# Optimization experiments

Hardware: AMD Instinct MI355X
Metric: run time of the kernel (lower is better)

The kernel has to match this reference:

```python
import jax, jax.numpy as jnp
import numpy as np

B, N, D = 8, 2048, 1024
A_STDP, TAU_STDP, W_OFF, T_MAX = 0.9, 0.5, 0.9, 1.0
V_TH, EPS = 1.0, 1e-5


def setup_inputs() -> dict:
    key = jax.random.key(0)
    ks = jax.random.split(key, 6)
    s = 0.02
    inp = {"x": jax.random.normal(ks[0], (B, N, D), dtype=jnp.float32)}
    for i, nm in enumerate(["q", "k", "v"]):
        inp[f"W{nm}"] = jax.random.normal(ks[1 + i], (D, D), dtype=jnp.float32) * s
        inp[f"g{nm}"] = jnp.ones((D,), jnp.float32)
        inp[f"b{nm}"] = jnp.zeros((D,), jnp.float32)
        inp[f"m{nm}"] = jnp.zeros((D,), jnp.float32)
        inp[f"v{nm}"] = jnp.ones((D,), jnp.float32)
    inp["Wo"] = jax.random.normal(ks[4], (D, D), dtype=jnp.float32) * s
    inp["bo"] = jnp.zeros((D,), jnp.float32)
    return inp


def _proj(x, W, g, b, m, v):
    # Linear (no bias) -> BatchNorm1d (inference, running stats) -> LIF first step
    h = x @ W                                     # [B,N,D]
    h = (h - m) * (g * jax.lax.rsqrt(v + EPS)) + b
    # LIF with mem=None: mem = x, spike = sigmoid(4*(mem - v_th))
    return jax.nn.sigmoid(4.0 * (h - V_TH))


def reference(x, Wq, gq, bq, mq, vq, Wk, gk, bk, mk, vk, Wv, gv, bv, mv, vv, Wo, bo):
    Q = _proj(x, Wq, gq, bq, mq, vq)
    K = _proj(x, Wk, gk, bk, mk, vk)
    V = _proj(x, Wv, gv, bv, mv, vv)
    t_Q = T_MAX * (1.0 - Q.mean(axis=-1, keepdims=True))   # [B,N,1]
    t_K = T_MAX * (1.0 - K.mean(axis=-1, keepdims=True))   # [B,N,1]
    delta_t = t_Q - jnp.swapaxes(t_K, 1, 2)                 # [B,N,N]
    f_stdp = A_STDP * jnp.exp(-jnp.abs(delta_t) / TAU_STDP)
    A = jnp.where(delta_t < 0, f_stdp, -f_stdp) + W_OFF     # [B,N,N]
    return (A @ V) @ Wo + bo                                # [B,N,D]
```

## Files before the change

kernel.cpp:

```cpp
#include <hip/hip_runtime.h>

#define B_ 8
#define N_ 2048
#define D_ 1024
#define M_ (B_*N_)
#define SEGS 64
#define EPB (4096/SEGS)
#define CW 256

typedef __attribute__((ext_vector_type(8))) short short8;
typedef __attribute__((ext_vector_type(4))) float floatx4;

__device__ __forceinline__ ushort f2bf(float f) {
  unsigned u = __builtin_bit_cast(unsigned, f);
  return (ushort)((u + 0x7fffu + ((u >> 16) & 1u)) >> 16);
}
__device__ __forceinline__ float bf2f(ushort u) {
  return __builtin_bit_cast(float, ((unsigned)u) << 16);
}
__device__ __forceinline__ void gload16(const void* g, void* l) {
  __builtin_amdgcn_global_load_lds(
      (const __attribute__((address_space(1))) unsigned*)g,
      (__attribute__((address_space(3))) unsigned*)l, 16, 0, 0);
}
__device__ __forceinline__ float sig4(float h) {
  return 1.0f / (1.0f + __expf(4.0f - 4.0f*h));
}

__global__ __launch_bounds__(256) void conv_x_k(const float4* __restrict__ x,
                                                ushort4* __restrict__ o) {
  int i = blockIdx.x * 256 + threadIdx.x;
  float4 f = x[i];
  ushort4 u;
  u.x = f2bf(f.x); u.y = f2bf(f.y); u.z = f2bf(f.z); u.w = f2bf(f.w);
  o[i] = u;
}

__global__ __launch_bounds__(256) void transpose_k(
    const float* __restrict__ Wq, const float* __restrict__ Wk,
    const float* __restrict__ Wv, const float* __restrict__ Wo,
    ushort* __restrict__ W3T, ushort* __restrict__ WoT) {
  __shared__ float tile[32][33];
  int z = blockIdx.z;
  const float* W = (z == 0) ? Wq : (z == 1) ? Wk : (z == 2) ? Wv : Wo;
  ushort* WT = (z < 3) ? (W3T + (size_t)z * D_ * D_) : WoT;
  int tx = threadIdx.x, ty = threadIdx.y;
  int x = blockIdx.x * 32 + tx;
  int y = blockIdx.y * 32 + ty;
#pragma unroll
  for (int j = 0; j < 32; j += 8)
    tile[ty + j][tx] = W[(size_t)(y + j) * D_ + x];
  __syncthreads();
  int x2 = blockIdx.y * 32 + tx;
  int y2 = blockIdx.x * 32 + ty;
#pragma unroll
  for (int j = 0; j < 32; j += 8)
    WT[(size_t)(y2 + j) * D_ + x2] = f2bf(tile[tx][ty + j]);
}

__device__ __forceinline__ void mainloop256(
    const ushort* __restrict__ Ab, const ushort* __restrict__ Bb,
    ushort* __restrict__ As, ushort* __restrict__ Bs, int t,
    floatx4 (&acc)[8][4])
{
  const int lane = t & 63, wid = t >> 6;
  const int quad = lane >> 4, l15 = lane & 15;
  const int wm = wid >> 2, wn = wid & 3;

  int srcO[2], dsto[2];
#pragma unroll
  for (int r = 0; r < 2; r++) {
    int li = r * 512 + t;
    int row = li >> 2, c = li & 3;
    int soff = ((c - (row >> 1)) & 3) * 8;
    srcO[r] = row * D_ + soff;
    dsto[r] = li * 16;
  }

  int offA[8], offB[4];
#pragma unroll
  for (int i = 0; i < 8; i++) {
    int row = wm * 128 + i * 16 + l15;
    offA[i] = row * 32 + ((quad + (row >> 1)) & 3) * 8;
  }
#pragma unroll
  for (int i = 0; i < 4; i++) {
    int row = wn * 64 + i * 16 + l15;
    offB[i] = row * 32 + ((quad + (row >> 1)) & 3) * 8;
  }

#pragma unroll
  for (int pt = 0; pt < 3; pt++) {
#pragma unroll
    for (int r = 0; r < 2; r++)
      gload16(Ab + srcO[r] + pt * 32, (char*)(As + pt * 8192) + dsto[r]);
#pragma unroll
    for (int r = 0; r < 2; r++)
      gload16(Bb + srcO[r] + pt * 32, (char*)(Bs + pt * 8192) + dsto[r]);
  }

  const int NT = D_ / 32;
#pragma unroll 4
  for (int tt = 0; tt < NT; tt++) {
    if (tt < NT - 2)       asm volatile("s_waitcnt vmcnt(8)" ::: "memory");
    else if (tt == NT - 2) asm volatile("s_waitcnt vmcnt(4)" ::: "memory");
    else                   asm volatile("s_waitcnt vmcnt(0)" ::: "memory");
    __builtin_amdgcn_s_barrier();
    const ushort* Asl = As + (tt & 3) * 8192;
    const ushort* Bsl = Bs + (tt & 3) * 8192;
    const bool pf = (tt + 3 < NT);

    short8 af[4], bfr[4];
#pragma unroll
    for (int i = 0; i < 4; i++) af[i] = *(const short8*)(Asl + offA[i]);
#pragma unroll
    for (int i = 0; i < 4; i++) bfr[i] = *(const short8*)(Bsl + offB[i]);
    if (pf) {
      ushort* d = As + ((tt + 3) & 3) * 8192;
#pragma unroll
      for (int r = 0; r < 2; r++)
        gload16(Ab + srcO[r] + (tt + 3) * 32, (char*)d + dsto[r]);
    }
    __builtin_amdgcn_s_barrier();
    __builtin_amdgcn_sched_barrier(0);
    __builtin_amdgcn_s_setprio(1);
#pragma unroll
    for (int tm = 0; tm < 4; tm++)
#pragma unroll
      for (int tn = 0; tn < 4; tn++)
        acc[tm][tn] = __builtin_amdgcn_mfma_f32_16x16x32_bf16(
            af[tm], bfr[tn], acc[tm][tn], 0, 0, 0);
    __builtin_amdgcn_s_setprio(0);

    short8 ag[4];
#pragma unroll
    for (int i = 0; i < 4; i++) ag[i] = *(const short8*)(Asl + offA[4 + i]);
    if (pf) {
      ushort* d = Bs + ((tt + 3) & 3) * 8192;
#pragma unroll
      for (int r = 0; r < 2; r++)
        gload16(Bb + srcO[r] + (tt + 3) * 32, (char*)d + dsto[r]);
    }
    __builtin_amdgcn_s_barrier();
    __builtin_amdgcn_sched_barrier(0);
    __builtin_amdgcn_s_setprio(1);
#pragma unroll
    for (int tm = 0; tm < 4; tm++)
#pragma unroll
      for (int tn = 0; tn < 4; tn++)
        acc[4 + tm][tn] = __builtin_amdgcn_mfma_f32_16x16x32_bf16(
            ag[tm], bfr[tn], acc[4 + tm][tn], 0, 0, 0);
    __builtin_amdgcn_s_setprio(0);
  }
}

__global__ __launch_bounds__(512, 2) void gemm_qkv_k(
    const ushort* __restrict__ A, const ushort* __restrict__ W3T,
    const float* __restrict__ gq, const float* __restrict__ bq,
    const float* __restrict__ mq, const float* __restrict__ vq,
    const float* __restrict__ gk, const float* __restrict__ bk,
    const float* __restrict__ mk, const float* __restrict__ vk,
    const float* __restrict__ gv, const float* __restrict__ bv,
    const float* __restrict__ mv, const float* __restrict__ vv,
    float* __restrict__ rsQ, float* __restrict__ rsK, ushort* __restrict__ Vb)
{
  __shared__ ushort As[4 * 8192];
  __shared__ ushort Bs[4 * 8192];
  const int t = threadIdx.x;
  const int lane = t & 63, wid = t >> 6;
  const int quad = lane >> 4, l15 = lane & 15;
  const int wm = wid >> 2, wn = wid & 3;

  const int lin = blockIdx.x;
  const int xcd = lin & 7, s = lin >> 3;
  const int z = s >> 5;
  const int rem = s & 31;
  const int mg = rem >> 2;
  const int nt = rem & 3;
  const int tileM = (xcd * 8 + mg) * 256;
  const int tileN = nt * 256;

  const float* gg  = (z == 0) ? gq : (z == 1) ? gk : gv;
  const float* bb  = (z == 0) ? bq : (z == 1) ? bk : bv;
  const float* mmn = (z == 0) ? mq : (z == 1) ? mk : mv;
  const float* vvn = (z == 0) ? vq : (z == 1) ? vk : vv;

  float sc[4], sh[4];
#pragma unroll
  for (int tn = 0; tn < 4; tn++) {
    int col = tileN + wn * 64 + tn * 16 + l15;
    float scv = gg[col] * rsqrtf(vvn[col] + 1e-5f);
    sc[tn] = scv;
    sh[tn] = bb[col] - mmn[col] * scv;
  }
  asm volatile("s_waitcnt vmcnt(0)" ::: "memory");

  floatx4 acc[8][4];
#pragma unroll
  for (int i = 0; i < 8; i++)
#pragma unroll
    for (int j = 0; j < 4; j++) acc[i][j] = (floatx4){0.f, 0.f, 0.f, 0.f};

  mainloop256(A + (size_t)tileM * D_,
              W3T + (size_t)z * D_ * D_ + (size_t)tileN * D_,
              As, Bs, t, acc);

  if (z == 2) {
#pragma unroll
    for (int tm = 0; tm < 8; tm++) {
      int row0 = tileM + wm * 128 + tm * 16 + quad * 4;
#pragma unroll
      for (int tn = 0; tn < 4; tn++) {
        int col = tileN + wn * 64 + tn * 16 + l15;
#pragma unroll
        for (int r = 0; r < 4; r++)
          Vb[(size_t)(row0 + r) * D_ + col] =
              f2bf(sig4(acc[tm][tn][r] * sc[tn] + sh[tn]));
      }
    }
  } else {
    float* rowsum = (z == 0) ? rsQ : rsK;
#pragma unroll
    for (int tm = 0; tm < 8; tm++) {
      float rs[4] = {0.f, 0.f, 0.f, 0.f};
#pragma unroll
      for (int tn = 0; tn < 4; tn++)
#pragma unroll
        for (int r = 0; r < 4; r++)
          rs[r] += sig4(acc[tm][tn][r] * sc[tn] + sh[tn]);
#pragma unroll
      for (int off = 1; off < 16; off <<= 1)
#pragma unroll
        for (int r = 0; r < 4; r++)
          rs[r] += __shfl_xor(rs[r], off, 64);
      if (l15 == 0) {
        int row0 = tileM + wm * 128 + tm * 16 + quad * 4;
#pragma unroll
        for (int r = 0; r < 4; r++)
          atomicAdd(&rowsum[row0 + r], rs[r]);
      }
    }
  }
}

__global__ __launch_bounds__(512, 2) void gemm_out_k(
    const ushort* __restrict__ A, const ushort* __restrict__ Bt,
    float* __restrict__ outF, const float* __restrict__ bo)
{
  __shared__ ushort As[4 * 8192];
  __shared__ ushort Bs[4 * 8192];
  const int t = threadIdx.x;
  const int lane = t & 63, wid = t >> 6;
  const int quad = lane >> 4, l15 = lane & 15;
  const int wm = wid >> 2, wn = wid & 3;

  const int lin = blockIdx.x;
  const int xcd = lin & 7, s = lin >> 3;
  const int mg = s >> 2, nt = s & 3;
  const int tileM = (xcd * 8 + mg) * 256;
  const int tileN = nt * 256;

  float bias[4];
#pragma unroll
  for (int tn = 0; tn < 4; tn++)
    bias[tn] = bo[tileN + wn * 64 + tn * 16 + l15];
  asm volatile("s_waitcnt vmcnt(0)" ::: "memory");

  floatx4 acc[8][4];
#pragma unroll
  for (int i = 0; i < 8; i++)
#pragma unroll
    for (int j = 0; j < 4; j++) acc[i][j] = (floatx4){0.f, 0.f, 0.f, 0.f};

  mainloop256(A + (size_t)tileM * D_, Bt + (size_t)tileN * D_, As, Bs, t, acc);

#pragma unroll
  for (int tm = 0; tm < 8; tm++) {
    int row0 = tileM + wm * 128 + tm * 16 + quad * 4;
#pragma unroll
    for (int tn = 0; tn < 4; tn++) {
      int col = tileN + wn * 64 + tn * 16 + l15;
#pragma unroll
      for (int r = 0; r < 4; r++)
        outF[(size_t)(row0 + r) * D_ + col] = acc[tm][tn][r] + bias[tn];
    }
  }
}

__global__ __launch_bounds__(256) void rank_events_k(
    const float* __restrict__ rsQ, const float* __restrict__ rsK,
    int* __restrict__ evt_tag, float* __restrict__ evt_wa, float* __restrict__ evt_wd)
{
  __shared__ unsigned long long keys[4096];
  __shared__ int part[256];
  int b = blockIdx.y, chunk = blockIdx.x;
  int t = threadIdx.x;
  for (int i = t; i < 4096; i += 256) {
    float v; unsigned tag;
    if (i < 2048) {
      v = 1.0f - rsQ[b * N_ + i] * (1.0f / 1024.0f);
      tag = (unsigned)i | 0x10000u;
    } else {
      int j = i - 2048;
      v = 1.0f - rsK[b * N_ + j] * (1.0f / 1024.0f);
      tag = (unsigned)j;
    }
    keys[i] = ((unsigned long long)__builtin_bit_cast(unsigned, v) << 32) | tag;
  }
  __syncthreads();
  int e = chunk * 128 + (t & 127);
  int j0 = (t >> 7) * 2048;
  unsigned long long me = keys[e];
  int r = 0;
#pragma unroll 8
  for (int j = 0; j < 2048; j++) r += (keys[j0 + j] < me) ? 1 : 0;
  part[t] = r;
  __syncthreads();
  if (t < 128) {
    int rank = part[t] + part[t + 128];
    unsigned tag = (unsigned)(me & 0x1FFFFu);
    float v = __builtin_bit_cast(float, (unsigned)(me >> 32));
    bool isq = (tag & 0x10000u) != 0;
    int o = b * 4096 + rank;
    evt_tag[o] = (int)tag;
    evt_wa[o] = isq ? expf(-2.0f * v) : expf(2.0f * v);
    evt_wd[o] = isq ? expf(2.0f * v) : expf(-2.0f * v);
  }
}

__global__ __launch_bounds__(256) void seg_tot_k(
    const int* __restrict__ evt_tag, const float* __restrict__ evt_wa,
    const float* __restrict__ evt_wd, const ushort* __restrict__ Vb,
    float* __restrict__ totWA, float* __restrict__ totWD, float* __restrict__ totP)
{
  __shared__ int srow[EPB];
  __shared__ float swa[EPB], swd[EPB], spw[EPB];
  int b = blockIdx.z, seg = blockIdx.y, chunk = blockIdx.x;
  int t = threadIdx.x;
  int e0 = b * 4096 + seg * EPB;
  if (t < EPB) {
    int tg = evt_tag[e0 + t];
    bool isk = !(tg & 0x10000);
    srow[t] = isk ? (tg & 0xFFFF) : 0;
    swa[t] = isk ? evt_wa[e0 + t] : 0.f;
    swd[t] = isk ? evt_wd[e0 + t] : 0.f;
    spw[t] = isk ? 1.f : 0.f;
  }
  __syncthreads();
  int c = chunk * 512 + t * 2;
  const ushort* vb = Vb + (size_t)b * N_ * D_ + c;
  float wa0 = 0, wa1 = 0, wd0 = 0, wd1 = 0, p0 = 0, p1 = 0;
#pragma unroll 8
  for (int e = 0; e < EPB; e++) {
    unsigned raw = *(const unsigned*)(vb + (size_t)srow[e] * D_);
    float v0 = bf2f((ushort)(raw & 0xffffu)), v1 = bf2f((ushort)(raw >> 16));
    float wa = swa[e], wd = swd[e], pw = spw[e];
    wa0 += wa * v0; wa1 += wa * v1;
    wd0 += wd * v0; wd1 += wd * v1;
    p0 += pw * v0;  p1 += pw * v1;
  }
  size_t o = ((size_t)b * SEGS + seg) * D_ + c;
  totWA[o] = wa0; totWA[o + 1] = wa1;
  totWD[o] = wd0; totWD[o + 1] = wd1;
  totP[o]  = p0;  totP[o + 1]  = p1;
}

__global__ __launch_bounds__(256) void seg_prefix_k(
    const float* __restrict__ totWA, const float* __restrict__ totWD,
    const float* __restrict__ totP,
    float* __restrict__ preA, float* __restrict__ prePA,
    float* __restrict__ sufD, float* __restrict__ sufPD)
{
  int b = blockIdx.y;
  int c = blockIdx.x * 256 + threadIdx.x;
  float a = 0, pa = 0;
  for (int s = 0; s < SEGS; s++) {
    size_t o = ((size_t)b * SEGS + s) * D_ + c;
    preA[o] = a; prePA[o] = pa;
    a += totWA[o]; pa += totP[o];
  }
  float d = 0, pd = 0;
  for (int s = SEGS - 1; s >= 0; s--) {
    size_t o = ((size_t)b * SEGS + s) * D_ + c;
    sufD[o] = d; sufPD[o] = pd;
    d += totWD[o]; pd += totP[o];
  }
}

__global__ __launch_bounds__(256) void scan_both_k(
    const int* __restrict__ evt_tag, const float* __restrict__ evt_wa,
    const float* __restrict__ evt_wd, const ushort* __restrict__ Vb,
    const float* __restrict__ preA, const float* __restrict__ prePA,
    const float* __restrict__ sufD, const float* __restrict__ sufPD,
    float* AVpart, ushort* __restrict__ AVb)
{
  __shared__ ushort Vt[EPB * CW];
  __shared__ int sisq[EPB], sidx[EPB];
  __shared__ float skwa[EPB], skwd[EPB], sqwa[EPB], sqwd[EPB], spk[EPB];
  int b = blockIdx.z, seg = blockIdx.y, chunk = blockIdx.x;
  int t = threadIdx.x;
  int e0 = b * 4096 + seg * EPB;
  if (t < EPB) {
    int tg = evt_tag[e0 + t];
    bool isq = (tg & 0x10000) != 0;
    float wa = evt_wa[e0 + t], wd = evt_wd[e0 + t];
    sisq[t] = isq; sidx[t] = isq ? (tg & 0xFFFF) : 0;
    skwa[t] = isq ? 0.f : wa;  sqwa[t] = wa;
    skwd[t] = isq ? 0.f : wd;  sqwd[t] = wd;
    spk[t]  = isq ? 0.f : 1.f;
  }
  __syncthreads();
  int c0 = chunk * CW;
  const ushort* vbase = Vb + (size_t)b * N_ * D_ + c0;
  __shared__ int srow[EPB];
  if (t < EPB) {
    int tg = evt_tag[e0 + t];
    srow[t] = (tg & 0x10000) ? 0 : (tg & 0xFFFF);
  }
  __syncthreads();
#pragma unroll
  for (int r = 0; r < 8; r++) {
    int li = r * 256 + t;
    int e = li >> 5, ch = li & 31;
    gload16(vbase + (size_t)srow[e] * D_ + ch * 8, (char*)Vt + li * 16);
  }
  __syncthreads();

  int cth = c0 + t;
  size_t po = ((size_t)b * SEGS + seg) * D_ + cth;
  float* AVrow = AVpart + (size_t)b * N_ * D_ + cth;
  ushort* AVbrow = AVb + (size_t)b * N_ * D_ + cth;

  {
    float s = preA[po], p = prePA[po];
#pragma unroll 4
    for (int e = 0; e < EPB; e++) {
      float v = bf2f(Vt[e * CW + t]);
      if (sisq[e]) AVrow[(size_t)sidx[e] * D_] = 0.9f * (p - sqwa[e] * s);
      s += skwa[e] * v; p += spk[e] * v;
    }
  }
  {
    float s = sufD[po], p = sufPD[po];
#pragma unroll 4
    for (int e = EPB - 1; e >= 0; e--) {
      float v = bf2f(Vt[e * CW + t]);
      if (sisq[e]) {
        size_t o = (size_t)sidx[e] * D_;
        AVbrow[o] = f2bf(AVrow[o] + 0.9f * (p + sqwd[e] * s));
      }
      s += skwd[e] * v; p += spk[e] * v;
    }
  }
}

extern "C" void kernel_launch(void* const* d_in, const int* in_sizes, int n_in,
                              void* d_out, int out_size, void* d_ws, size_t ws_size,
                              hipStream_t stream) {
  (void)in_sizes; (void)n_in; (void)out_size; (void)ws_size;
  const float* x  = (const float*)d_in[0];
  const float* Wq = (const float*)d_in[1];
  const float* gq = (const float*)d_in[2];
  const float* bq = (const float*)d_in[3];
  const float* mq = (const float*)d_in[4];
  const float* vq = (const float*)d_in[5];
  const float* Wk = (const float*)d_in[6];
  const float* gk = (const float*)d_in[7];
  const float* bk = (const float*)d_in[8];
  const float* mk = (const float*)d_in[9];
  const float* vk = (const float*)d_in[10];
  const float* Wv = (const float*)d_in[11];
  const float* gv = (const float*)d_in[12];
  const float* bv = (const float*)d_in[13];
  const float* mv = (const float*)d_in[14];
  const float* vv = (const float*)d_in[15];
  const float* Wo = (const float*)d_in[16];
  const float* bo = (const float*)d_in[17];

  char* p = (char*)d_ws;
  auto alloc = [&](size_t n) { char* r = p; p += n; return r; };
  ushort* x16  = (ushort*)alloc((size_t)M_ * D_ * 2);
  ushort* Vb   = (ushort*)alloc((size_t)M_ * D_ * 2);
  ushort* AVb  = (ushort*)alloc((size_t)M_ * D_ * 2);
  ushort* W3T  = (ushort*)alloc((size_t)3 * D_ * D_ * 2);
  ushort* WoT  = (ushort*)alloc((size_t)D_ * D_ * 2);
  float*  rsQ  = (float*)alloc((size_t)M_ * 4);
  float*  rsK  = (float*)alloc((size_t)M_ * 4);
  int*    evt_tag = (int*)alloc((size_t)B_ * 4096 * 4);
  float*  evt_wa  = (float*)alloc((size_t)B_ * 4096 * 4);
  float*  evt_wd  = (float*)alloc((size_t)B_ * 4096 * 4);
  float*  totWA   = (float*)alloc((size_t)B_ * SEGS * D_ * 4);
  float*  totWD   = (float*)alloc((size_t)B_ * SEGS * D_ * 4);
  float*  totP    = (float*)alloc((size_t)B_ * SEGS * D_ * 4);
  float*  preA    = (float*)alloc((size_t)B_ * SEGS * D_ * 4);
  float*  prePA   = (float*)alloc((size_t)B_ * SEGS * D_ * 4);
  float*  sufD    = (float*)alloc((size_t)B_ * SEGS * D_ * 4);
  float*  sufPD   = (float*)alloc((size_t)B_ * SEGS * D_ * 4);

  hipMemsetAsync(rsQ, 0, (size_t)2 * M_ * 4, stream);

  conv_x_k<<<(M_ * D_) / 1024, 256, 0, stream>>>((const float4*)x, (ushort4*)x16);
  dim3 tb(32, 8), tg(32, 32, 4);
  transpose_k<<<tg, tb, 0, stream>>>(Wq, Wk, Wv, Wo, W3T, WoT);

  gemm_qkv_k<<<768, 512, 0, stream>>>(x16, W3T, gq, bq, mq, vq,
                                      gk, bk, mk, vk, gv, bv, mv, vv,
                                      rsQ, rsK, Vb);

  rank_events_k<<<dim3(32, B_), 256, 0, stream>>>(rsQ, rsK, evt_tag, evt_wa, evt_wd);

  seg_tot_k<<<dim3(2, SEGS, B_), 256, 0, stream>>>(evt_tag, evt_wa, evt_wd, Vb,
                                                   totWA, totWD, totP);
  seg_prefix_k<<<dim3(D_ / 256, B_), 256, 0, stream>>>(totWA, totWD, totP,
                                                       preA, prePA, sufD, sufPD);
  scan_both_k<<<dim3(D_ / CW, SEGS, B_), 256, 0, stream>>>(
      evt_tag, evt_wa, evt_wd, Vb, preA, prePA, sufD, sufPD, (float*)d_out, AVb);

  gemm_out_k<<<256, 512, 0, stream>>>(AVb, WoT, (float*)d_out, bo);
}
```

Baseline: 435.9 us.

## Software-pipeline LDS fragment loads across k-steps and drop one barrier per iteration

Restructures the shared GEMM mainloop so the A and B fragments for the next k-step are read from LDS during the current step's second MFMA half. B fragments ping-pong between two register sets, and A and B global prefetches are issued together. This removes one of the two barriers per k-iteration and loosens the vmcnt waits. The epilogue parameter loads (BN scale/shift, bias) move after the mainloop so they no longer need an explicit vmcnt(0) before it starts. The cost is extra live registers at 2 waves/SIMD and a subtler correctness reliance on lgkmcnt/vmcnt counts.

```diff
diff --git a/kernel.cpp b/kernel.cpp
--- a/kernel.cpp
+++ b/kernel.cpp
@@ -99,29 +99,33 @@
       gload16(Bb + srcO[r] + pt * 32, (char*)(Bs + pt * 8192) + dsto[r]);
   }
 
+  short8 a03[4], a47[4], bE[4], bO[4];
+
+  asm volatile("s_waitcnt vmcnt(4)" ::: "memory");
+  __builtin_amdgcn_s_barrier();
+#pragma unroll
+  for (int i = 0; i < 4; i++) a03[i] = *(const short8*)(As + offA[i]);
+#pragma unroll
+  for (int i = 0; i < 4; i++) bE[i]  = *(const short8*)(Bs + offB[i]);
+
   const int NT = D_ / 32;
-#pragma unroll 4
-  for (int tt = 0; tt < NT; tt++) {
-    if (tt < NT - 2)       asm volatile("s_waitcnt vmcnt(8)" ::: "memory");
-    else if (tt == NT - 2) asm volatile("s_waitcnt vmcnt(4)" ::: "memory");
-    else                   asm volatile("s_waitcnt vmcnt(0)" ::: "memory");
+
+  auto kstep = [&](int k, short8 (&bCur)[4], short8 (&bNxt)[4]) {
+    if (k < NT - 2) asm volatile("s_waitcnt vmcnt(4) lgkmcnt(8)" ::: "memory");
+    else            asm volatile("s_waitcnt vmcnt(0) lgkmcnt(8)" ::: "memory");
     __builtin_amdgcn_s_barrier();
-    const ushort* Asl = As + (tt & 3) * 8192;
-    const ushort* Bsl = Bs + (tt & 3) * 8192;
-    const bool pf = (tt + 3 < NT);
-
-    short8 af[4], bfr[4];
-#pragma unroll
-    for (int i = 0; i < 4; i++) af[i] = *(const short8*)(Asl + offA[i]);
-#pragma unroll
-    for (int i = 0; i < 4; i++) bfr[i] = *(const short8*)(Bsl + offB[i]);
-    if (pf) {
-      ushort* d = As + ((tt + 3) & 3) * 8192;
-#pragma unroll
-      for (int r = 0; r < 2; r++)
-        gload16(Ab + srcO[r] + (tt + 3) * 32, (char*)d + dsto[r]);
-    }
-    __builtin_amdgcn_s_barrier();
+    const ushort* Asl = As + (k & 3) * 8192;
+#pragma unroll
+    for (int i = 0; i < 4; i++) a47[i] = *(const short8*)(Asl + offA[4 + i]);
+    if (k + 3 < NT) {
+      ushort* dA = As + ((k + 3) & 3) * 8192;
+      ushort* dB = Bs + ((k + 3) & 3) * 8192;
+#pragma unroll
+      for (int r = 0; r < 2; r++) {
+        gload16(Ab + srcO[r] + (k + 3) * 32, (char*)dA + dsto[r]);
+        gload16(Bb + srcO[r] + (k + 3) * 32, (char*)dB + dsto[r]);
+      }
+    }
     __builtin_amdgcn_sched_barrier(0);
     __builtin_amdgcn_s_setprio(1);
 #pragma unroll
@@ -129,19 +133,17 @@
 #pragma unroll
       for (int tn = 0; tn < 4; tn++)
         acc[tm][tn] = __builtin_amdgcn_mfma_f32_16x16x32_bf16(
-            af[tm], bfr[tn], acc[tm][tn], 0, 0, 0);
+            a03[tm], bCur[tn], acc[tm][tn], 0, 0, 0);
     __builtin_amdgcn_s_setprio(0);
-
-    short8 ag[4];
-#pragma unroll
-    for (int i = 0; i < 4; i++) ag[i] = *(const short8*)(Asl + offA[4 + i]);
-    if (pf) {
-      ushort* d = Bs + ((tt + 3) & 3) * 8192;
-#pragma unroll
-      for (int r = 0; r < 2; r++)
-        gload16(Bb + srcO[r] + (tt + 3) * 32, (char*)d + dsto[r]);
-    }
-    __builtin_amdgcn_s_barrier();
+    __builtin_amdgcn_sched_barrier(0);
+    if (k + 1 < NT) {
+      const ushort* Asl2 = As + ((k + 1) & 3) * 8192;
+      const ushort* Bsl2 = Bs + ((k + 1) & 3) * 8192;
+#pragma unroll
+      for (int i = 0; i < 4; i++) a03[i] = *(const short8*)(Asl2 + offA[i]);
+#pragma unroll
+      for (int i = 0; i < 4; i++) bNxt[i] = *(const short8*)(Bsl2 + offB[i]);
+    }
     __builtin_amdgcn_sched_barrier(0);
     __builtin_amdgcn_s_setprio(1);
 #pragma unroll
@@ -149,8 +151,13 @@
 #pragma unroll
       for (int tn = 0; tn < 4; tn++)
         acc[4 + tm][tn] = __builtin_amdgcn_mfma_f32_16x16x32_bf16(
-            ag[tm], bfr[tn], acc[4 + tm][tn], 0, 0, 0);
+            a47[tm], bCur[tn], acc[4 + tm][tn], 0, 0, 0);
     __builtin_amdgcn_s_setprio(0);
+  };
+
+  for (int k = 0; k < NT; k += 2) {
+    kstep(k,     bE, bO);
+    kstep(k + 1, bO, bE);
   }
 }
 
@@ -180,11 +187,20 @@
   const int tileM = (xcd * 8 + mg) * 256;
   const int tileN = nt * 256;
 
+  floatx4 acc[8][4];
+#pragma unroll
+  for (int i = 0; i < 8; i++)
+#pragma unroll
+    for (int j = 0; j < 4; j++) acc[i][j] = (floatx4){0.f, 0.f, 0.f, 0.f};
+
+  mainloop256(A + (size_t)tileM * D_,
+              W3T + (size_t)z * D_ * D_ + (size_t)tileN * D_,
+              As, Bs, t, acc);
+
   const float* gg  = (z == 0) ? gq : (z == 1) ? gk : gv;
   const float* bb  = (z == 0) ? bq : (z == 1) ? bk : bv;
   const float* mmn = (z == 0) ? mq : (z == 1) ? mk : mv;
   const float* vvn = (z == 0) ? vq : (z == 1) ? vk : vv;
-
   float sc[4], sh[4];
 #pragma unroll
   for (int tn = 0; tn < 4; tn++) {
@@ -193,17 +209,6 @@
     sc[tn] = scv;
     sh[tn] = bb[col] - mmn[col] * scv;
   }
-  asm volatile("s_waitcnt vmcnt(0)" ::: "memory");
-
-  floatx4 acc[8][4];
-#pragma unroll
-  for (int i = 0; i < 8; i++)
-#pragma unroll
-    for (int j = 0; j < 4; j++) acc[i][j] = (floatx4){0.f, 0.f, 0.f, 0.f};
-
-  mainloop256(A + (size_t)tileM * D_,
-              W3T + (size_t)z * D_ * D_ + (size_t)tileN * D_,
-              As, Bs, t, acc);
 
   if (z == 2) {
 #pragma unroll
@@ -260,12 +265,6 @@
   const int tileM = (xcd * 8 + mg) * 256;
   const int tileN = nt * 256;
 
-  float bias[4];
-#pragma unroll
-  for (int tn = 0; tn < 4; tn++)
-    bias[tn] = bo[tileN + wn * 64 + tn * 16 + l15];
-  asm volatile("s_waitcnt vmcnt(0)" ::: "memory");
-
   floatx4 acc[8][4];
 #pragma unroll
   for (int i = 0; i < 8; i++)
@@ -275,14 +274,15 @@
   mainloop256(A + (size_t)tileM * D_, Bt + (size_t)tileN * D_, As, Bs, t, acc);
 
 #pragma unroll
-  for (int tm = 0; tm < 8; tm++) {
-    int row0 = tileM + wm * 128 + tm * 16 + quad * 4;
-#pragma unroll
-    for (int tn = 0; tn < 4; tn++) {
-      int col = tileN + wn * 64 + tn * 16 + l15;
+  for (int tn = 0; tn < 4; tn++) {
+    int col = tileN + wn * 64 + tn * 16 + l15;
+    float bias = bo[col];
+#pragma unroll
+    for (int tm = 0; tm < 8; tm++) {
+      int row0 = tileM + wm * 128 + tm * 16 + quad * 4;
 #pragma unroll
       for (int r = 0; r < 4; r++)
-        outF[(size_t)(row0 + r) * D_ + col] = acc[tm][tn][r] + bias[tn];
+        outF[(size_t)(row0 + r) * D_ + col] = acc[tm][tn][r] + bias;
     }
   }
 }
```

New measurement: 438.5 us. Within noise of the previous version (+0.6%).

## Merge forward and backward segment scans into one pass using total V sum

Applied to the files above, without the earlier changes.

Rewrites the per-query output so the ±f term splits into a forward prefix of wa-weighted V, a suffix of wd-weighted V taken as total minus a running prefix, and a constant 0.9·ΣV offset. This lets a single forward pass over each segment's events produce the result. It drops the prePA/sufPD arrays, the fp32 scratch round trip through d_out, and the second scan loop. seg_prefix_k now keeps the 64 segment totals in registers, which may raise register pressure. Rounding can differ slightly because the suffix is computed by subtraction.

```diff
diff --git a/kernel.cpp b/kernel.cpp
--- a/kernel.cpp
+++ b/kernel.cpp
@@ -368,35 +368,50 @@
 __global__ __launch_bounds__(256) void seg_prefix_k(
     const float* __restrict__ totWA, const float* __restrict__ totWD,
     const float* __restrict__ totP,
-    float* __restrict__ preA, float* __restrict__ prePA,
-    float* __restrict__ sufD, float* __restrict__ sufPD)
+    float* __restrict__ preA, float* __restrict__ sufD,
+    float* __restrict__ Vsum)
 {
   int b = blockIdx.y;
   int c = blockIdx.x * 256 + threadIdx.x;
-  float a = 0, pa = 0;
+  size_t base = (size_t)b * SEGS * D_ + c;
+
+  float va[SEGS];
+  float psum = 0.f;
+#pragma unroll
   for (int s = 0; s < SEGS; s++) {
-    size_t o = ((size_t)b * SEGS + s) * D_ + c;
-    preA[o] = a; prePA[o] = pa;
-    a += totWA[o]; pa += totP[o];
-  }
-  float d = 0, pd = 0;
+    va[s] = totWA[base + (size_t)s * D_];
+    psum += totP[base + (size_t)s * D_];
+  }
+  Vsum[b * D_ + c] = psum;
+  float a = 0.f;
+#pragma unroll
+  for (int s = 0; s < SEGS; s++) {
+    preA[base + (size_t)s * D_] = a;
+    a += va[s];
+  }
+
+  float vd[SEGS];
+#pragma unroll
+  for (int s = 0; s < SEGS; s++)
+    vd[s] = totWD[base + (size_t)s * D_];
+  float d = 0.f;
+#pragma unroll
   for (int s = SEGS - 1; s >= 0; s--) {
-    size_t o = ((size_t)b * SEGS + s) * D_ + c;
-    sufD[o] = d; sufPD[o] = pd;
-    d += totWD[o]; pd += totP[o];
-  }
-}
-
-__global__ __launch_bounds__(256) void scan_both_k(
+    sufD[base + (size_t)s * D_] = d;
+    d += vd[s];
+  }
+}
+
+__global__ __launch_bounds__(256) void scan_one_k(
     const int* __restrict__ evt_tag, const float* __restrict__ evt_wa,
     const float* __restrict__ evt_wd, const ushort* __restrict__ Vb,
-    const float* __restrict__ preA, const float* __restrict__ prePA,
-    const float* __restrict__ sufD, const float* __restrict__ sufPD,
-    float* AVpart, ushort* __restrict__ AVb)
+    const float* __restrict__ preA, const float* __restrict__ sufD,
+    const float* __restrict__ totWD, const float* __restrict__ Vsum,
+    ushort* __restrict__ AVb)
 {
   __shared__ ushort Vt[EPB * CW];
-  __shared__ int sisq[EPB], sidx[EPB];
-  __shared__ float skwa[EPB], skwd[EPB], sqwa[EPB], sqwd[EPB], spk[EPB];
+  __shared__ int sisq[EPB], sidx[EPB], srow[EPB];
+  __shared__ float skwa[EPB], skwd[EPB], sqwa[EPB], sqwd[EPB];
   int b = blockIdx.z, seg = blockIdx.y, chunk = blockIdx.x;
   int t = threadIdx.x;
   int e0 = b * 4096 + seg * EPB;
@@ -405,19 +420,13 @@
     bool isq = (tg & 0x10000) != 0;
     float wa = evt_wa[e0 + t], wd = evt_wd[e0 + t];
     sisq[t] = isq; sidx[t] = isq ? (tg & 0xFFFF) : 0;
+    srow[t] = isq ? 0 : (tg & 0xFFFF);
     skwa[t] = isq ? 0.f : wa;  sqwa[t] = wa;
     skwd[t] = isq ? 0.f : wd;  sqwd[t] = wd;
-    spk[t]  = isq ? 0.f : 1.f;
   }
   __syncthreads();
   int c0 = chunk * CW;
   const ushort* vbase = Vb + (size_t)b * N_ * D_ + c0;
-  __shared__ int srow[EPB];
-  if (t < EPB) {
-    int tg = evt_tag[e0 + t];
-    srow[t] = (tg & 0x10000) ? 0 : (tg & 0xFFFF);
-  }
-  __syncthreads();
 #pragma unroll
   for (int r = 0; r < 8; r++) {
     int li = r * 256 + t;
@@ -428,29 +437,21 @@
 
   int cth = c0 + t;
   size_t po = ((size_t)b * SEGS + seg) * D_ + cth;
-  float* AVrow = AVpart + (size_t)b * N_ * D_ + cth;
+  float sA   = preA[po];
+  float sD0  = sufD[po] + totWD[po];
+  float voff = 0.9f * Vsum[b * D_ + cth];
+  float sDacc = 0.f;
   ushort* AVbrow = AVb + (size_t)b * N_ * D_ + cth;
 
-  {
-    float s = preA[po], p = prePA[po];
 #pragma unroll 4
-    for (int e = 0; e < EPB; e++) {
-      float v = bf2f(Vt[e * CW + t]);
-      if (sisq[e]) AVrow[(size_t)sidx[e] * D_] = 0.9f * (p - sqwa[e] * s);
-      s += skwa[e] * v; p += spk[e] * v;
-    }
-  }
-  {
-    float s = sufD[po], p = sufPD[po];
-#pragma unroll 4
-    for (int e = EPB - 1; e >= 0; e--) {
-      float v = bf2f(Vt[e * CW + t]);
-      if (sisq[e]) {
-        size_t o = (size_t)sidx[e] * D_;
-        AVbrow[o] = f2bf(AVrow[o] + 0.9f * (p + sqwd[e] * s));
-      }
-      s += skwd[e] * v; p += spk[e] * v;
-    }
+  for (int e = 0; e < EPB; e++) {
+    float v = bf2f(Vt[e * CW + t]);
+    if (sisq[e]) {
+      float out = voff + 0.9f * (sqwd[e] * (sD0 - sDacc) - sqwa[e] * sA);
+      AVbrow[(size_t)sidx[e] * D_] = f2bf(out);
+    }
+    sA    += skwa[e] * v;
+    sDacc += skwd[e] * v;
   }
 }
 
@@ -493,9 +494,8 @@
   float*  totWD   = (float*)alloc((size_t)B_ * SEGS * D_ * 4);
   float*  totP    = (float*)alloc((size_t)B_ * SEGS * D_ * 4);
   float*  preA    = (float*)alloc((size_t)B_ * SEGS * D_ * 4);
-  float*  prePA   = (float*)alloc((size_t)B_ * SEGS * D_ * 4);
   float*  sufD    = (float*)alloc((size_t)B_ * SEGS * D_ * 4);
-  float*  sufPD   = (float*)alloc((size_t)B_ * SEGS * D_ * 4);
+  float*  VsumW   = (float*)alloc((size_t)B_ * D_ * 4);
 
   hipMemsetAsync(rsQ, 0, (size_t)2 * M_ * 4, stream);
 
@@ -512,9 +512,9 @@
   seg_tot_k<<<dim3(2, SEGS, B_), 256, 0, stream>>>(evt_tag, evt_wa, evt_wd, Vb,
                                                    totWA, totWD, totP);
   seg_prefix_k<<<dim3(D_ / 256, B_), 256, 0, stream>>>(totWA, totWD, totP,
-                                                       preA, prePA, sufD, sufPD);
-  scan_both_k<<<dim3(D_ / CW, SEGS, B_), 256, 0, stream>>>(
-      evt_tag, evt_wa, evt_wd, Vb, preA, prePA, sufD, sufPD, (float*)d_out, AVb);
+                                                       preA, sufD, VsumW);
+  scan_one_k<<<dim3(D_ / CW, SEGS, B_), 256, 0, stream>>>(
+      evt_tag, evt_wa, evt_wd, Vb, preA, sufD, totWD, VsumW, AVb);
 
   gemm_out_k<<<256, 512, 0, stream>>>(AVb, WoT, (float*)d_out, bo);
 }
```

Result: faster. 397.0 us (-8.9%).
